# Performance work log

Hardware: AMD Instinct MI355X
Metric: run time of the kernel (lower is better)

## Reference

```python
import jax, jax.numpy as jnp
import numpy as np

N_NODES = 10000
EPS = 1e-5


def _layernorm(x, gamma, beta):
    mu = jnp.mean(x, axis=-1, keepdims=True)
    var = jnp.mean(jnp.square(x - mu), axis=-1, keepdims=True)
    return (x - mu) * jax.lax.rsqrt(var + EPS) * gamma + beta


def _sage_pool_layer(h, src, dst, Wp, bp, Ws, Wn, b, gamma, beta):
    # DGL SAGEConv(aggregator='pool'):
    #   m_u = relu(h_u @ Wp^T + bp); h_neigh[v] = max_{u in N(v)} m_u (0 if no neighbors)
    #   rst = h @ Ws^T + h_neigh @ Wn^T + b
    m = jax.nn.relu(h @ Wp.T + bp)              # [N, d]
    msg = m[src]                                 # [E, d] gather
    agg = jax.ops.segment_max(msg, dst, num_segments=N_NODES)
    agg = jnp.where(jnp.isfinite(agg), agg, 0.0)  # isolated nodes -> 0
    rst = h @ Ws.T + agg @ Wn.T + b
    # gsage_layer: LayerNorm, then Encoder applies relu (dropout inactive in eval)
    return jax.nn.relu(_layernorm(rst, gamma, beta))


def setup_inputs() -> dict:
    key = jax.random.key(0)
    ks = jax.random.split(key, 16)
    d = 256
    E = 320000
    s = 1.0 / np.sqrt(d)
    inp = {
        "h": jax.random.normal(ks[0], (N_NODES, d), dtype=jnp.float32),
        "edge_src": jax.random.randint(ks[1], (E,), 0, N_NODES, dtype=jnp.int32),
        "edge_dst": jax.random.randint(ks[2], (E,), 0, N_NODES, dtype=jnp.int32),
    }
    for li in range(2):
        kk = jax.random.split(ks[3 + li], 3)
        inp[f"Wp{li}"] = jax.random.normal(kk[0], (d, d), dtype=jnp.float32) * s
        inp[f"bp{li}"] = jnp.zeros((d,), jnp.float32)
        inp[f"Ws{li}"] = jax.random.normal(kk[1], (d, d), dtype=jnp.float32) * s
        inp[f"Wn{li}"] = jax.random.normal(kk[2], (d, d), dtype=jnp.float32) * s
        inp[f"b{li}"] = jnp.zeros((d,), jnp.float32)
        inp[f"g{li}"] = jnp.ones((d,), jnp.float32)
        inp[f"be{li}"] = jnp.zeros((d,), jnp.float32)
    return inp


def reference(h, edge_src, edge_dst,
              Wp0, bp0, Ws0, Wn0, b0, g0, be0,
              Wp1, bp1, Ws1, Wn1, b1, g1, be1):
    h = _sage_pool_layer(h, edge_src, edge_dst, Wp0, bp0, Ws0, Wn0, b0, g0, be0)
    h = _sage_pool_layer(h, edge_src, edge_dst, Wp1, bp1, Ws1, Wn1, b1, g1, be1)
    return h
```

## Files before the change

### kernel.cpp

```cpp
#include <hip/hip_runtime.h>

#define D 256
#define CAP 128
#define ASTRIDE 280
#define LN_EPS 1e-5f
#define MQ_ENC 32.0f
#define MQ_DEC 0.03125f

typedef short short8 __attribute__((ext_vector_type(8)));
typedef float floatx4 __attribute__((ext_vector_type(4)));
typedef unsigned short u16x8 __attribute__((ext_vector_type(8)));
typedef unsigned short us2 __attribute__((ext_vector_type(2)));

__device__ __forceinline__ unsigned short f2b(float f) {
    union { float f; unsigned int u; } x; x.f = f;
    unsigned int u = x.u + 0x7FFFu + ((x.u >> 16) & 1u);
    return (unsigned short)(u >> 16);
}

__device__ __forceinline__ unsigned bmax4(unsigned a, unsigned b) {
    union { unsigned u; us2 v; } al, bl, ah, bh, rl, rh;
    al.u = a & 0x00FF00FFu; bl.u = b & 0x00FF00FFu;
    ah.u = a & 0xFF00FF00u; bh.u = b & 0xFF00FF00u;
#if __has_builtin(__builtin_elementwise_max)
    rl.v = __builtin_elementwise_max(al.v, bl.v);
    rh.v = __builtin_elementwise_max(ah.v, bh.v);
#else
    rl.v[0] = al.v[0] > bl.v[0] ? al.v[0] : bl.v[0];
    rl.v[1] = al.v[1] > bl.v[1] ? al.v[1] : bl.v[1];
    rh.v[0] = ah.v[0] > bh.v[0] ? ah.v[0] : bh.v[0];
    rh.v[1] = ah.v[1] > bh.v[1] ? ah.v[1] : bh.v[1];
#endif
    return rl.u | rh.u;
}

__device__ __forceinline__ uint2 bmax8(uint2 a, uint2 b) {
    uint2 r; r.x = bmax4(a.x, b.x); r.y = bmax4(a.y, b.y); return r;
}

__device__ __forceinline__ unsigned char mq(float v) {
    return (unsigned char)(int)fminf(v * MQ_ENC + 0.5f, 255.0f);
}

__device__ __forceinline__ u16x8 deq8(uint2 x) {
    u16x8 r;
#pragma unroll
    for (int k = 0; k < 2; k++) {
        const unsigned w = k ? x.y : x.x;
#pragma unroll
        for (int j = 0; j < 4; j++)
            r[k * 4 + j] = f2b((float)((w >> (8 * j)) & 0xFFu) * MQ_DEC);
    }
    return r;
}

__global__ __launch_bounds__(256) void prep_kernel(
    const float* __restrict__ w0, const float* __restrict__ w1,
    const float* __restrict__ w2, const float* __restrict__ w3,
    const float* __restrict__ w4, const float* __restrict__ w5,
    unsigned short* __restrict__ wb,
    int* __restrict__ cnt, unsigned char* __restrict__ mb8,
    unsigned char* __restrict__ m1b8, int N)
{
    const int blk = blockIdx.x;
    const int tid = threadIdx.x;
    if (blk < 384) {
        const int wsel = blk >> 6;
        const float* src;
        switch (wsel) {
            case 0: src = w0; break; case 1: src = w1; break;
            case 2: src = w2; break; case 3: src = w3; break;
            case 4: src = w4; break; default: src = w5; break;
        }
        const int idx = (blk & 63) * 1024 + tid * 4;
        const float4 v = *(const float4*)(src + idx);
        ushort4 o;
        o.x = f2b(v.x); o.y = f2b(v.y); o.z = f2b(v.z); o.w = f2b(v.w);
        *(ushort4*)(wb + (size_t)wsel * 65536 + idx) = o;
    } else if (blk < 424) {
        const int i = (blk - 384) * 256 + tid;
        if (i < N) cnt[i] = 0;
    } else {
        mb8[(size_t)N * D + tid] = 0;
        m1b8[(size_t)N * D + tid] = 0;
    }
}

__global__ __launch_bounds__(256, 3) void relu_m(
    const float* __restrict__ h, const unsigned short* __restrict__ Wp,
    const float* __restrict__ bp, unsigned char* __restrict__ mb8,
    unsigned short* __restrict__ hb, int N,
    const int* __restrict__ esrc, const int* __restrict__ edst,
    int* __restrict__ cnt, unsigned short* __restrict__ csr, int E, int ngemm)
{
    if ((int)blockIdx.x >= ngemm) {
        const int nsb = gridDim.x - ngemm;
        int i = ((int)blockIdx.x - ngemm) * 256 + threadIdx.x;
        const int stride = nsb * 256;
        for (; i < E; i += stride) {
            const int d = edst[i];
            const int pos = atomicAdd(&cnt[d], 1);
            if (pos < CAP) csr[(size_t)d * CAP + pos] = (unsigned short)esrc[i];
        }
        return;
    }

    const int tid = threadIdx.x;
    const int wave = tid >> 6;
    const int lane = tid & 63;
    const int quad = lane >> 4;
    const int l16 = lane & 15;
    const int row0 = blockIdx.x * 16;
    const int koff = quad * 8;

    floatx4 acc[4];
#pragma unroll
    for (int t = 0; t < 4; t++) acc[t] = (floatx4)(0.f);

    const float* aptr = h + (size_t)(row0 + l16) * D + koff;
    const unsigned short* wptr = Wp + (size_t)(wave * 64 + l16) * D + koff;
#pragma unroll
    for (int k0 = 0; k0 < D; k0 += 32) {
        const float4 f0 = *(const float4*)(aptr + k0);
        const float4 f1 = *(const float4*)(aptr + k0 + 4);
        union { short8 s; ushort4 h[2]; } av;
        av.h[0].x = f2b(f0.x); av.h[0].y = f2b(f0.y);
        av.h[0].z = f2b(f0.z); av.h[0].w = f2b(f0.w);
        av.h[1].x = f2b(f1.x); av.h[1].y = f2b(f1.y);
        av.h[1].z = f2b(f1.z); av.h[1].w = f2b(f1.w);
        if (wave == 0)
            *(short8*)(hb + (size_t)(row0 + l16) * D + koff + k0) = av.s;
        const short8 b0 = *(const short8*)(wptr + k0);
        const short8 b1 = *(const short8*)(wptr + 16 * D + k0);
        const short8 b2 = *(const short8*)(wptr + 32 * D + k0);
        const short8 b3 = *(const short8*)(wptr + 48 * D + k0);
        acc[0] = __builtin_amdgcn_mfma_f32_16x16x32_bf16(av.s, b0, acc[0], 0, 0, 0);
        acc[1] = __builtin_amdgcn_mfma_f32_16x16x32_bf16(av.s, b1, acc[1], 0, 0, 0);
        acc[2] = __builtin_amdgcn_mfma_f32_16x16x32_bf16(av.s, b2, acc[2], 0, 0, 0);
        acc[3] = __builtin_amdgcn_mfma_f32_16x16x32_bf16(av.s, b3, acc[3], 0, 0, 0);
    }

#pragma unroll
    for (int t = 0; t < 4; t++) {
        const float bcol = bp[wave * 64 + t * 16 + l16];
#pragma unroll
        for (int r = 0; r < 4; r++) {
            const int rg = row0 + quad * 4 + r;
            const int col = wave * 64 + t * 16 + l16;
            mb8[(size_t)rg * D + col] = mq(fmaxf(acc[t][r] + bcol, 0.f));
        }
    }
}

__global__ __launch_bounds__(256, 3) void gemm_ln_pool(
    const unsigned short* __restrict__ A, const unsigned short* __restrict__ Wself,
    const unsigned short* __restrict__ Wneigh,
    const unsigned char* __restrict__ mpool,
    const int* __restrict__ cnt, const unsigned short* __restrict__ csr,
    const float* __restrict__ bias,
    const float* __restrict__ gamma, const float* __restrict__ beta,
    unsigned short* __restrict__ out_b, float* __restrict__ out_f,
    const unsigned short* __restrict__ Wnext, const float* __restrict__ bnext,
    unsigned char* __restrict__ mout, int N)
{
    __shared__ unsigned short idxS[16][CAP];
    __shared__ unsigned short aggS[16 * ASTRIDE];
    __shared__ float redS[4][16], redS2[4][16], muA[16], rsA[16];

    const int tid = threadIdx.x;
    const int wave = tid >> 6;
    const int lane = tid & 63;
    const int quad = lane >> 4;
    const int l16 = lane & 15;
    const int row0 = blockIdx.x * 16;
    const int koff = quad * 8;
    const int rbase = wave * 4;
    const int half = lane >> 5;
    const int l32 = lane & 31;

    int degs[4];
#pragma unroll
    for (int rr = 0; rr < 4; rr++) degs[rr] = min(cnt[row0 + rbase + rr], CAP);
    int P = max(max(degs[0], degs[1]), max(degs[2], degs[3]));
    const int P2R = (P + 7) & ~7;
#pragma unroll
    for (int rr = 0; rr < 4; rr++) {
        const int rg = row0 + rbase + rr;
        for (int i = lane; i < P2R; i += 64)
            idxS[rbase + rr][i] = (i < degs[rr]) ? csr[(size_t)rg * CAP + i]
                                                 : (unsigned short)N;
    }

    const int nb = P2R >> 1;
    const unsigned char* mbase = mpool + l32 * 8;

#define ISSUE_B(SL, bi)                                                         \
    {                                                                           \
        _Pragma("unroll") for (int rr = 0; rr < 4; rr++) {                      \
            const int jj = idxS[rbase + rr][2 * (bi) + half];                   \
            SL[rr] = *(const uint2*)(mbase + (size_t)jj * D);                   \
        }                                                                       \
    }
#define CONS_B(SL)                                                              \
    {                                                                           \
        _Pragma("unroll") for (int rr = 0; rr < 4; rr++)                        \
            mx[rr] = bmax8(mx[rr], SL[rr]);                                     \
    }

    uint2 g0[4], g1[4], g2[4], g3[4], mx[4];
#pragma unroll
    for (int rr = 0; rr < 4; rr++) mx[rr] = make_uint2(0u, 0u);

    if (nb) {
        ISSUE_B(g0, 0) ISSUE_B(g1, 1) ISSUE_B(g2, 2) ISSUE_B(g3, 3)
    }

    floatx4 acc[4];
#pragma unroll
    for (int t = 0; t < 4; t++) acc[t] = (floatx4)(0.f);

    {
        const unsigned short* aptr = A + (size_t)(row0 + l16) * D + koff;
        const unsigned short* wptr = Wself + (size_t)(wave * 64 + l16) * D + koff;
#pragma unroll
        for (int k0 = 0; k0 < D; k0 += 32) {
            const short8 av = *(const short8*)(aptr + k0);
            const short8 b0 = *(const short8*)(wptr + k0);
            const short8 b1 = *(const short8*)(wptr + 16 * D + k0);
            const short8 b2 = *(const short8*)(wptr + 32 * D + k0);
            const short8 b3 = *(const short8*)(wptr + 48 * D + k0);
            acc[0] = __builtin_amdgcn_mfma_f32_16x16x32_bf16(av, b0, acc[0], 0, 0, 0);
            acc[1] = __builtin_amdgcn_mfma_f32_16x16x32_bf16(av, b1, acc[1], 0, 0, 0);
            acc[2] = __builtin_amdgcn_mfma_f32_16x16x32_bf16(av, b2, acc[2], 0, 0, 0);
            acc[3] = __builtin_amdgcn_mfma_f32_16x16x32_bf16(av, b3, acc[3], 0, 0, 0);
        }
    }

    for (int b = 0; b < nb; b += 4) {
        const bool more = (b + 8 <= nb);
        CONS_B(g0) if (more) ISSUE_B(g0, b + 4)
        CONS_B(g1) if (more) ISSUE_B(g1, b + 5)
        CONS_B(g2) if (more) ISSUE_B(g2, b + 6)
        CONS_B(g3) if (more) ISSUE_B(g3, b + 7)
    }
#undef ISSUE_B
#undef CONS_B

#pragma unroll
    for (int rr = 0; rr < 4; rr++) {
        uint2 oth;
        oth.x = __shfl_xor((int)mx[rr].x, 32);
        oth.y = __shfl_xor((int)mx[rr].y, 32);
        const uint2 mf = bmax8(mx[rr], oth);
        if (half == 0)
            *(u16x8*)&aggS[(rbase + rr) * ASTRIDE + l32 * 8] = deq8(mf);
    }
    __syncthreads();

    {
        const unsigned short* wptr = Wneigh + (size_t)(wave * 64 + l16) * D + koff;
#pragma unroll
        for (int k0 = 0; k0 < D; k0 += 32) {
            const short8 av = *(const short8*)&aggS[l16 * ASTRIDE + koff + k0];
            const short8 b0 = *(const short8*)(wptr + k0);
            const short8 b1 = *(const short8*)(wptr + 16 * D + k0);
            const short8 b2 = *(const short8*)(wptr + 32 * D + k0);
            const short8 b3 = *(const short8*)(wptr + 48 * D + k0);
            acc[0] = __builtin_amdgcn_mfma_f32_16x16x32_bf16(av, b0, acc[0], 0, 0, 0);
            acc[1] = __builtin_amdgcn_mfma_f32_16x16x32_bf16(av, b1, acc[1], 0, 0, 0);
            acc[2] = __builtin_amdgcn_mfma_f32_16x16x32_bf16(av, b2, acc[2], 0, 0, 0);
            acc[3] = __builtin_amdgcn_mfma_f32_16x16x32_bf16(av, b3, acc[3], 0, 0, 0);
        }
    }

    float bcol[4];
#pragma unroll
    for (int t = 0; t < 4; t++) bcol[t] = bias[wave * 64 + t * 16 + l16];
#pragma unroll
    for (int t = 0; t < 4; t++)
#pragma unroll
        for (int r = 0; r < 4; r++) acc[t][r] += bcol[t];

#pragma unroll
    for (int r = 0; r < 4; r++) {
        float s = 0.f, s2 = 0.f;
#pragma unroll
        for (int t = 0; t < 4; t++) {
            const float v = acc[t][r];
            s += v; s2 += v * v;
        }
        s += __shfl_xor(s, 1);  s2 += __shfl_xor(s2, 1);
        s += __shfl_xor(s, 2);  s2 += __shfl_xor(s2, 2);
        s += __shfl_xor(s, 4);  s2 += __shfl_xor(s2, 4);
        s += __shfl_xor(s, 8);  s2 += __shfl_xor(s2, 8);
        if (l16 == 0) {
            redS[wave][quad * 4 + r] = s;
            redS2[wave][quad * 4 + r] = s2;
        }
    }
    __syncthreads();
    if (tid < 16) {
        const float S  = redS[0][tid] + redS[1][tid] + redS[2][tid] + redS[3][tid];
        const float S2 = redS2[0][tid] + redS2[1][tid] + redS2[2][tid] + redS2[3][tid];
        const float mu = S * (1.f / D);
        float var = S2 * (1.f / D) - mu * mu;
        var = fmaxf(var, 0.f);
        muA[tid] = mu;
        rsA[tid] = rsqrtf(var + LN_EPS);
    }
    __syncthreads();

    float gcol[4], becol[4];
#pragma unroll
    for (int t = 0; t < 4; t++) {
        gcol[t] = gamma[wave * 64 + t * 16 + l16];
        becol[t] = beta[wave * 64 + t * 16 + l16];
    }
#pragma unroll
    for (int r = 0; r < 4; r++) {
        const int rl = quad * 4 + r;
        const int rg = row0 + rl;
        const float mu = muA[rl];
        const float rs = rsA[rl];
#pragma unroll
        for (int t = 0; t < 4; t++) {
            const int col = wave * 64 + t * 16 + l16;
            float o = (acc[t][r] - mu) * rs * gcol[t] + becol[t];
            o = fmaxf(o, 0.f);
            const unsigned short ob = f2b(o);
            if (out_f) out_f[(size_t)rg * D + col] = o;
            else       out_b[(size_t)rg * D + col] = ob;
            if (Wnext) aggS[rl * ASTRIDE + col] = ob;
        }
    }

    if (Wnext) {
        __syncthreads();
#pragma unroll
        for (int t = 0; t < 4; t++) acc[t] = (floatx4)(0.f);
        const unsigned short* wptr = Wnext + (size_t)(wave * 64 + l16) * D + koff;
#pragma unroll
        for (int k0 = 0; k0 < D; k0 += 32) {
            const short8 av = *(const short8*)&aggS[l16 * ASTRIDE + koff + k0];
            const short8 b0 = *(const short8*)(wptr + k0);
            const short8 b1 = *(const short8*)(wptr + 16 * D + k0);
            const short8 b2 = *(const short8*)(wptr + 32 * D + k0);
            const short8 b3 = *(const short8*)(wptr + 48 * D + k0);
            acc[0] = __builtin_amdgcn_mfma_f32_16x16x32_bf16(av, b0, acc[0], 0, 0, 0);
            acc[1] = __builtin_amdgcn_mfma_f32_16x16x32_bf16(av, b1, acc[1], 0, 0, 0);
            acc[2] = __builtin_amdgcn_mfma_f32_16x16x32_bf16(av, b2, acc[2], 0, 0, 0);
            acc[3] = __builtin_amdgcn_mfma_f32_16x16x32_bf16(av, b3, acc[3], 0, 0, 0);
        }
#pragma unroll
        for (int t = 0; t < 4; t++) {
            const float bc = bnext[wave * 64 + t * 16 + l16];
#pragma unroll
            for (int r = 0; r < 4; r++) {
                const int rg = row0 + quad * 4 + r;
                const int col = wave * 64 + t * 16 + l16;
                mout[(size_t)rg * D + col] = mq(fmaxf(acc[t][r] + bc, 0.f));
            }
        }
    }
}

extern "C" void kernel_launch(void* const* d_in, const int* in_sizes, int n_in,
                              void* d_out, int out_size, void* d_ws, size_t ws_size,
                              hipStream_t stream) {
    const float* h    = (const float*)d_in[0];
    const int*   esrc = (const int*)d_in[1];
    const int*   edst = (const int*)d_in[2];
    const float* Wp0  = (const float*)d_in[3];
    const float* bp0  = (const float*)d_in[4];
    const float* Ws0  = (const float*)d_in[5];
    const float* Wn0  = (const float*)d_in[6];
    const float* b0   = (const float*)d_in[7];
    const float* g0   = (const float*)d_in[8];
    const float* be0  = (const float*)d_in[9];
    const float* Wp1  = (const float*)d_in[10];
    const float* bp1  = (const float*)d_in[11];
    const float* Ws1  = (const float*)d_in[12];
    const float* Wn1  = (const float*)d_in[13];
    const float* b1   = (const float*)d_in[14];
    const float* g1   = (const float*)d_in[15];
    const float* be1  = (const float*)d_in[16];

    const int N = in_sizes[0] / D;
    const int E = in_sizes[1];
    const size_t ND = (size_t)N * D;

    unsigned short* hb  = (unsigned short*)d_ws;
    unsigned short* h1b = hb + ND;
    unsigned short* wb  = h1b + ND;
    int* cnt = (int*)(wb + 6 * 65536);
    unsigned short* csr = (unsigned short*)(cnt + N);
    unsigned char* mb8  = (unsigned char*)(csr + (size_t)N * CAP);
    unsigned char* m1b8 = mb8 + ND + D;

    unsigned short* wpb0 = wb + 0 * 65536;
    unsigned short* wsb0 = wb + 1 * 65536;
    unsigned short* wnb0 = wb + 2 * 65536;
    unsigned short* wpb1 = wb + 3 * 65536;
    unsigned short* wsb1 = wb + 4 * 65536;
    unsigned short* wnb1 = wb + 5 * 65536;

    const int gblocks = N / 16;
    const int sblocks = 1024;

    prep_kernel<<<425, 256, 0, stream>>>(Wp0, Ws0, Wn0, Wp1, Ws1, Wn1, wb,
                                         cnt, mb8, m1b8, N);

    relu_m<<<gblocks + sblocks, 256, 0, stream>>>(h, wpb0, bp0, mb8, hb, N,
                                                  esrc, edst, cnt, csr, E, gblocks);
    gemm_ln_pool<<<gblocks, 256, 0, stream>>>(hb, wsb0, wnb0, mb8, cnt, csr,
                                              b0, g0, be0, h1b, nullptr,
                                              wpb1, bp1, m1b8, N);

    gemm_ln_pool<<<gblocks, 256, 0, stream>>>(h1b, wsb1, wnb1, m1b8, cnt, csr,
                                              b1, g1, be1, nullptr, (float*)d_out,
                                              nullptr, nullptr, nullptr, N);
}
```

Baseline: 213.5 us.

## Fuse both SAGE layers into one persistent kernel with a grid barrier

After: 406.2 us. 90.3% more time.

```diff
diff --git a/kernel.cpp b/kernel.cpp
--- a/kernel.cpp
+++ b/kernel.cpp
@@ -60,7 +60,7 @@
     const float* __restrict__ w4, const float* __restrict__ w5,
     unsigned short* __restrict__ wb,
     int* __restrict__ cnt, unsigned char* __restrict__ mb8,
-    unsigned char* __restrict__ m1b8, int N)
+    unsigned char* __restrict__ m1b8, unsigned* __restrict__ bar, int N)
 {
     const int blk = blockIdx.x;
     const int tid = threadIdx.x;
@@ -83,6 +83,7 @@
     } else {
         mb8[(size_t)N * D + tid] = 0;
         m1b8[(size_t)N * D + tid] = 0;
+        if (tid == 0) *bar = 0u;
     }
 }
 
@@ -152,19 +153,23 @@
     }
 }
 
-__global__ __launch_bounds__(256, 3) void gemm_ln_pool(
-    const unsigned short* __restrict__ A, const unsigned short* __restrict__ Wself,
-    const unsigned short* __restrict__ Wneigh,
-    const unsigned char* __restrict__ mpool,
+__global__ __launch_bounds__(256, 3) void lnpool2(
+    const unsigned short* __restrict__ A0,
+    const unsigned short* __restrict__ Ws0, const unsigned short* __restrict__ Wn0,
+    const unsigned char* __restrict__ m0,
     const int* __restrict__ cnt, const unsigned short* __restrict__ csr,
-    const float* __restrict__ bias,
-    const float* __restrict__ gamma, const float* __restrict__ beta,
-    unsigned short* __restrict__ out_b, float* __restrict__ out_f,
-    const unsigned short* __restrict__ Wnext, const float* __restrict__ bnext,
-    unsigned char* __restrict__ mout, int N)
+    const float* __restrict__ b0v, const float* __restrict__ g0v,
+    const float* __restrict__ be0v,
+    const unsigned short* __restrict__ Wp1, const float* __restrict__ bp1v,
+    unsigned char* __restrict__ m1,
+    const unsigned short* __restrict__ Ws1, const unsigned short* __restrict__ Wn1,
+    const float* __restrict__ b1v, const float* __restrict__ g1v,
+    const float* __restrict__ be1v,
+    float* __restrict__ outf, unsigned* __restrict__ bar, int N)
 {
     __shared__ unsigned short idxS[16][CAP];
-    __shared__ unsigned short aggS[16 * ASTRIDE];
+    __shared__ unsigned short aggA[16 * ASTRIDE];
+    __shared__ unsigned short aggB[16 * ASTRIDE];
     __shared__ float redS[4][16], redS2[4][16], muA[16], rsA[16];
 
     const int tid = threadIdx.x;
@@ -190,15 +195,13 @@
             idxS[rbase + rr][i] = (i < degs[rr]) ? csr[(size_t)rg * CAP + i]
                                                  : (unsigned short)N;
     }
-
     const int nb = P2R >> 1;
-    const unsigned char* mbase = mpool + l32 * 8;
-
-#define ISSUE_B(SL, bi)                                                         \
+
+#define ISSUE_B(SRC, SL, bi)                                                    \
     {                                                                           \
         _Pragma("unroll") for (int rr = 0; rr < 4; rr++) {                      \
             const int jj = idxS[rbase + rr][2 * (bi) + half];                   \
-            SL[rr] = *(const uint2*)(mbase + (size_t)jj * D);                   \
+            SL[rr] = *(const uint2*)((SRC) + (size_t)jj * D + l32 * 8);         \
         }                                                                       \
     }
 #define CONS_B(SL)                                                              \
@@ -206,120 +209,107 @@
         _Pragma("unroll") for (int rr = 0; rr < 4; rr++)                        \
             mx[rr] = bmax8(mx[rr], SL[rr]);                                     \
     }
+#define POOL_CONSUME(SRC)                                                       \
+    for (int b = 0; b < nb; b += 4) {                                           \
+        const bool more = (b + 8 <= nb);                                        \
+        CONS_B(g0) if (more) ISSUE_B(SRC, g0, b + 4)                            \
+        CONS_B(g1) if (more) ISSUE_B(SRC, g1, b + 5)                            \
+        CONS_B(g2) if (more) ISSUE_B(SRC, g2, b + 6)                            \
+        CONS_B(g3) if (more) ISSUE_B(SRC, g3, b + 7)                            \
+    }
+#define POOL_PARK()                                                             \
+    _Pragma("unroll") for (int rr = 0; rr < 4; rr++) {                          \
+        uint2 oth;                                                              \
+        oth.x = __shfl_xor((int)mx[rr].x, 32);                                  \
+        oth.y = __shfl_xor((int)mx[rr].y, 32);                                  \
+        const uint2 mf = bmax8(mx[rr], oth);                                    \
+        if (half == 0)                                                          \
+            *(u16x8*)&aggA[(rbase + rr) * ASTRIDE + l32 * 8] = deq8(mf);        \
+    }
+#define GEMM_GLB(APTR, WMAT)                                                    \
+    {                                                                           \
+        const unsigned short* wptr = (WMAT) + (size_t)(wave * 64 + l16) * D + koff; \
+        _Pragma("unroll") for (int k0 = 0; k0 < D; k0 += 32) {                  \
+            const short8 av = *(const short8*)((APTR) + k0);                    \
+            const short8 b0 = *(const short8*)(wptr + k0);                      \
+            const short8 b1 = *(const short8*)(wptr + 16 * D + k0);             \
+            const short8 b2 = *(const short8*)(wptr + 32 * D + k0);             \
+            const short8 b3 = *(const short8*)(wptr + 48 * D + k0);             \
+            acc[0] = __builtin_amdgcn_mfma_f32_16x16x32_bf16(av, b0, acc[0], 0, 0, 0); \
+            acc[1] = __builtin_amdgcn_mfma_f32_16x16x32_bf16(av, b1, acc[1], 0, 0, 0); \
+            acc[2] = __builtin_amdgcn_mfma_f32_16x16x32_bf16(av, b2, acc[2], 0, 0, 0); \
+            acc[3] = __builtin_amdgcn_mfma_f32_16x16x32_bf16(av, b3, acc[3], 0, 0, 0); \
+        }                                                                       \
+    }
+#define GEMM_LDS(ABUF, WMAT)                                                    \
+    {                                                                           \
+        const unsigned short* wptr = (WMAT) + (size_t)(wave * 64 + l16) * D + koff; \
+        _Pragma("unroll") for (int k0 = 0; k0 < D; k0 += 32) {                  \
+            const short8 av = *(const short8*)&(ABUF)[l16 * ASTRIDE + koff + k0]; \
+            const short8 b0 = *(const short8*)(wptr + k0);                      \
+            const short8 b1 = *(const short8*)(wptr + 16 * D + k0);             \
+            const short8 b2 = *(const short8*)(wptr + 32 * D + k0);             \
+            const short8 b3 = *(const short8*)(wptr + 48 * D + k0);             \
+            acc[0] = __builtin_amdgcn_mfma_f32_16x16x32_bf16(av, b0, acc[0], 0, 0, 0); \
+            acc[1] = __builtin_amdgcn_mfma_f32_16x16x32_bf16(av, b1, acc[1], 0, 0, 0); \
+            acc[2] = __builtin_amdgcn_mfma_f32_16x16x32_bf16(av, b2, acc[2], 0, 0, 0); \
+            acc[3] = __builtin_amdgcn_mfma_f32_16x16x32_bf16(av, b3, acc[3], 0, 0, 0); \
+        }                                                                       \
+    }
+#define LN_REDUCE(GV, BEV)                                                      \
+    _Pragma("unroll") for (int r = 0; r < 4; r++) {                             \
+        float s = 0.f, s2 = 0.f;                                                \
+        _Pragma("unroll") for (int t = 0; t < 4; t++) {                         \
+            const float v = acc[t][r]; s += v; s2 += v * v;                     \
+        }                                                                       \
+        s += __shfl_xor(s, 1);  s2 += __shfl_xor(s2, 1);                        \
+        s += __shfl_xor(s, 2);  s2 += __shfl_xor(s2, 2);                        \
+        s += __shfl_xor(s, 4);  s2 += __shfl_xor(s2, 4);                        \
+        s += __shfl_xor(s, 8);  s2 += __shfl_xor(s2, 8);                        \
+        if (l16 == 0) { redS[wave][quad * 4 + r] = s; redS2[wave][quad * 4 + r] = s2; } \
+    }                                                                           \
+    __syncthreads();                                                            \
+    if (tid < 16) {                                                             \
+        const float S  = redS[0][tid] + redS[1][tid] + redS[2][tid] + redS[3][tid];   \
+        const float S2 = redS2[0][tid] + redS2[1][tid] + redS2[2][tid] + redS2[3][tid]; \
+        const float mu = S * (1.f / D);                                         \
+        float var = S2 * (1.f / D) - mu * mu;                                   \
+        var = fmaxf(var, 0.f);                                                  \
+        muA[tid] = mu; rsA[tid] = rsqrtf(var + LN_EPS);                         \
+    }                                                                           \
+    __syncthreads();                                                            \
+    float gcol[4], becol[4];                                                    \
+    _Pragma("unroll") for (int t = 0; t < 4; t++) {                             \
+        gcol[t] = (GV)[wave * 64 + t * 16 + l16];                               \
+        becol[t] = (BEV)[wave * 64 + t * 16 + l16];                             \
+    }
 
     uint2 g0[4], g1[4], g2[4], g3[4], mx[4];
 #pragma unroll
     for (int rr = 0; rr < 4; rr++) mx[rr] = make_uint2(0u, 0u);
 
-    if (nb) {
-        ISSUE_B(g0, 0) ISSUE_B(g1, 1) ISSUE_B(g2, 2) ISSUE_B(g3, 3)
-    }
+    if (nb) { ISSUE_B(m0, g0, 0) ISSUE_B(m0, g1, 1) ISSUE_B(m0, g2, 2) ISSUE_B(m0, g3, 3) }
 
     floatx4 acc[4];
 #pragma unroll
     for (int t = 0; t < 4; t++) acc[t] = (floatx4)(0.f);
 
-    {
-        const unsigned short* aptr = A + (size_t)(row0 + l16) * D + koff;
-        const unsigned short* wptr = Wself + (size_t)(wave * 64 + l16) * D + koff;
-#pragma unroll
-        for (int k0 = 0; k0 < D; k0 += 32) {
-            const short8 av = *(const short8*)(aptr + k0);
-            const short8 b0 = *(const short8*)(wptr + k0);
-            const short8 b1 = *(const short8*)(wptr + 16 * D + k0);
-            const short8 b2 = *(const short8*)(wptr + 32 * D + k0);
-            const short8 b3 = *(const short8*)(wptr + 48 * D + k0);
-            acc[0] = __builtin_amdgcn_mfma_f32_16x16x32_bf16(av, b0, acc[0], 0, 0, 0);
-            acc[1] = __builtin_amdgcn_mfma_f32_16x16x32_bf16(av, b1, acc[1], 0, 0, 0);
-            acc[2] = __builtin_amdgcn_mfma_f32_16x16x32_bf16(av, b2, acc[2], 0, 0, 0);
-            acc[3] = __builtin_amdgcn_mfma_f32_16x16x32_bf16(av, b3, acc[3], 0, 0, 0);
-        }
-    }
-
-    for (int b = 0; b < nb; b += 4) {
-        const bool more = (b + 8 <= nb);
-        CONS_B(g0) if (more) ISSUE_B(g0, b + 4)
-        CONS_B(g1) if (more) ISSUE_B(g1, b + 5)
-        CONS_B(g2) if (more) ISSUE_B(g2, b + 6)
-        CONS_B(g3) if (more) ISSUE_B(g3, b + 7)
-    }
-#undef ISSUE_B
-#undef CONS_B
-
-#pragma unroll
-    for (int rr = 0; rr < 4; rr++) {
-        uint2 oth;
-        oth.x = __shfl_xor((int)mx[rr].x, 32);
-        oth.y = __shfl_xor((int)mx[rr].y, 32);
-        const uint2 mf = bmax8(mx[rr], oth);
-        if (half == 0)
-            *(u16x8*)&aggS[(rbase + rr) * ASTRIDE + l32 * 8] = deq8(mf);
-    }
+    GEMM_GLB(A0 + (size_t)(row0 + l16) * D + koff, Ws0)
+    POOL_CONSUME(m0)
+    POOL_PARK()
     __syncthreads();
-
-    {
-        const unsigned short* wptr = Wneigh + (size_t)(wave * 64 + l16) * D + koff;
-#pragma unroll
-        for (int k0 = 0; k0 < D; k0 += 32) {
-            const short8 av = *(const short8*)&aggS[l16 * ASTRIDE + koff + k0];
-            const short8 b0 = *(const short8*)(wptr + k0);
-            const short8 b1 = *(const short8*)(wptr + 16 * D + k0);
-            const short8 b2 = *(const short8*)(wptr + 32 * D + k0);
-            const short8 b3 = *(const short8*)(wptr + 48 * D + k0);
-            acc[0] = __builtin_amdgcn_mfma_f32_16x16x32_bf16(av, b0, acc[0], 0, 0, 0);
-            acc[1] = __builtin_amdgcn_mfma_f32_16x16x32_bf16(av, b1, acc[1], 0, 0, 0);
-            acc[2] = __builtin_amdgcn_mfma_f32_16x16x32_bf16(av, b2, acc[2], 0, 0, 0);
-            acc[3] = __builtin_amdgcn_mfma_f32_16x16x32_bf16(av, b3, acc[3], 0, 0, 0);
-        }
-    }
-
-    float bcol[4];
-#pragma unroll
-    for (int t = 0; t < 4; t++) bcol[t] = bias[wave * 64 + t * 16 + l16];
-#pragma unroll
-    for (int t = 0; t < 4; t++)
-#pragma unroll
-        for (int r = 0; r < 4; r++) acc[t][r] += bcol[t];
-
-#pragma unroll
-    for (int r = 0; r < 4; r++) {
-        float s = 0.f, s2 = 0.f;
-#pragma unroll
-        for (int t = 0; t < 4; t++) {
-            const float v = acc[t][r];
-            s += v; s2 += v * v;
-        }
-        s += __shfl_xor(s, 1);  s2 += __shfl_xor(s2, 1);
-        s += __shfl_xor(s, 2);  s2 += __shfl_xor(s2, 2);
-        s += __shfl_xor(s, 4);  s2 += __shfl_xor(s2, 4);
-        s += __shfl_xor(s, 8);  s2 += __shfl_xor(s2, 8);
-        if (l16 == 0) {
-            redS[wave][quad * 4 + r] = s;
-            redS2[wave][quad * 4 + r] = s2;
-        }
-    }
-    __syncthreads();
-    if (tid < 16) {
-        const float S  = redS[0][tid] + redS[1][tid] + redS[2][tid] + redS[3][tid];
-        const float S2 = redS2[0][tid] + redS2[1][tid] + redS2[2][tid] + redS2[3][tid];
-        const float mu = S * (1.f / D);
-        float var = S2 * (1.f / D) - mu * mu;
-        var = fmaxf(var, 0.f);
-        muA[tid] = mu;
-        rsA[tid] = rsqrtf(var + LN_EPS);
-    }
-    __syncthreads();
-
-    float gcol[4], becol[4];
+    GEMM_LDS(aggA, Wn0)
+
 #pragma unroll
     for (int t = 0; t < 4; t++) {
-        gcol[t] = gamma[wave * 64 + t * 16 + l16];
-        becol[t] = beta[wave * 64 + t * 16 + l16];
-    }
+        const float bc = b0v[wave * 64 + t * 16 + l16];
+#pragma unroll
+        for (int r = 0; r < 4; r++) acc[t][r] += bc;
+    }
+    LN_REDUCE(g0v, be0v)
 #pragma unroll
     for (int r = 0; r < 4; r++) {
         const int rl = quad * 4 + r;
-        const int rg = row0 + rl;
         const float mu = muA[rl];
         const float rs = rsA[rl];
 #pragma unroll
@@ -327,41 +317,78 @@
             const int col = wave * 64 + t * 16 + l16;
             float o = (acc[t][r] - mu) * rs * gcol[t] + becol[t];
             o = fmaxf(o, 0.f);
-            const unsigned short ob = f2b(o);
-            if (out_f) out_f[(size_t)rg * D + col] = o;
-            else       out_b[(size_t)rg * D + col] = ob;
-            if (Wnext) aggS[rl * ASTRIDE + col] = ob;
-        }
-    }
-
-    if (Wnext) {
-        __syncthreads();
-#pragma unroll
-        for (int t = 0; t < 4; t++) acc[t] = (floatx4)(0.f);
-        const unsigned short* wptr = Wnext + (size_t)(wave * 64 + l16) * D + koff;
-#pragma unroll
-        for (int k0 = 0; k0 < D; k0 += 32) {
-            const short8 av = *(const short8*)&aggS[l16 * ASTRIDE + koff + k0];
-            const short8 b0 = *(const short8*)(wptr + k0);
-            const short8 b1 = *(const short8*)(wptr + 16 * D + k0);
-            const short8 b2 = *(const short8*)(wptr + 32 * D + k0);
-            const short8 b3 = *(const short8*)(wptr + 48 * D + k0);
-            acc[0] = __builtin_amdgcn_mfma_f32_16x16x32_bf16(av, b0, acc[0], 0, 0, 0);
-            acc[1] = __builtin_amdgcn_mfma_f32_16x16x32_bf16(av, b1, acc[1], 0, 0, 0);
-            acc[2] = __builtin_amdgcn_mfma_f32_16x16x32_bf16(av, b2, acc[2], 0, 0, 0);
-            acc[3] = __builtin_amdgcn_mfma_f32_16x16x32_bf16(av, b3, acc[3], 0, 0, 0);
-        }
-#pragma unroll
-        for (int t = 0; t < 4; t++) {
-            const float bc = bnext[wave * 64 + t * 16 + l16];
-#pragma unroll
-            for (int r = 0; r < 4; r++) {
-                const int rg = row0 + quad * 4 + r;
+            aggB[rl * ASTRIDE + col] = f2b(o);
+        }
+    }
+    __syncthreads();
+
+#pragma unroll
+    for (int t = 0; t < 4; t++) acc[t] = (floatx4)(0.f);
+    GEMM_LDS(aggB, Wp1)
+#pragma unroll
+    for (int t = 0; t < 4; t++) {
+        const float bc = bp1v[wave * 64 + t * 16 + l16];
+#pragma unroll
+        for (int r = 0; r < 4; r++) {
+            const int rg = row0 + quad * 4 + r;
+            const int col = wave * 64 + t * 16 + l16;
+            m1[(size_t)rg * D + col] = mq(fmaxf(acc[t][r] + bc, 0.f));
+        }
+    }
+
+    __syncthreads();
+    if (tid == 0) {
+        __threadfence();
+        __hip_atomic_fetch_add(bar, 1u, __ATOMIC_ACQ_REL, __HIP_MEMORY_SCOPE_AGENT);
+        while (__hip_atomic_load(bar, __ATOMIC_ACQUIRE, __HIP_MEMORY_SCOPE_AGENT)
+               < (unsigned)gridDim.x)
+            __builtin_amdgcn_s_sleep(16);
+    }
+    __syncthreads();
+    __threadfence();
+
+#pragma unroll
+    for (int rr = 0; rr < 4; rr++) mx[rr] = make_uint2(0u, 0u);
+    if (nb) { ISSUE_B(m1, g0, 0) ISSUE_B(m1, g1, 1) ISSUE_B(m1, g2, 2) ISSUE_B(m1, g3, 3) }
+
+#pragma unroll
+    for (int t = 0; t < 4; t++) acc[t] = (floatx4)(0.f);
+
+    GEMM_LDS(aggB, Ws1)
+    POOL_CONSUME(m1)
+    POOL_PARK()
+    __syncthreads();
+    GEMM_LDS(aggA, Wn1)
+
+#pragma unroll
+    for (int t = 0; t < 4; t++) {
+        const float bc = b1v[wave * 64 + t * 16 + l16];
+#pragma unroll
+        for (int r = 0; r < 4; r++) acc[t][r] += bc;
+    }
+    {
+        LN_REDUCE(g1v, be1v)
+#pragma unroll
+        for (int r = 0; r < 4; r++) {
+            const int rl = quad * 4 + r;
+            const int rg = row0 + rl;
+            const float mu = muA[rl];
+            const float rs = rsA[rl];
+#pragma unroll
+            for (int t = 0; t < 4; t++) {
                 const int col = wave * 64 + t * 16 + l16;
-                mout[(size_t)rg * D + col] = mq(fmaxf(acc[t][r] + bc, 0.f));
+                float o = (acc[t][r] - mu) * rs * gcol[t] + becol[t];
+                outf[(size_t)rg * D + col] = fmaxf(o, 0.f);
             }
         }
     }
+#undef ISSUE_B
+#undef CONS_B
+#undef POOL_CONSUME
+#undef POOL_PARK
+#undef GEMM_GLB
+#undef GEMM_LDS
+#undef LN_REDUCE
 }
 
 extern "C" void kernel_launch(void* const* d_in, const int* in_sizes, int n_in,
@@ -390,12 +417,12 @@
     const size_t ND = (size_t)N * D;
 
     unsigned short* hb  = (unsigned short*)d_ws;
-    unsigned short* h1b = hb + ND;
-    unsigned short* wb  = h1b + ND;
+    unsigned short* wb  = hb + ND;
     int* cnt = (int*)(wb + 6 * 65536);
     unsigned short* csr = (unsigned short*)(cnt + N);
     unsigned char* mb8  = (unsigned char*)(csr + (size_t)N * CAP);
     unsigned char* m1b8 = mb8 + ND + D;
+    unsigned* bar = (unsigned*)(m1b8 + ND + D);
 
     unsigned short* wpb0 = wb + 0 * 65536;
     unsigned short* wsb0 = wb + 1 * 65536;
@@ -408,15 +435,13 @@
     const int sblocks = 1024;
 
     prep_kernel<<<425, 256, 0, stream>>>(Wp0, Ws0, Wn0, Wp1, Ws1, Wn1, wb,
-                                         cnt, mb8, m1b8, N);
+                                         cnt, mb8, m1b8, bar, N);
 
     relu_m<<<gblocks + sblocks, 256, 0, stream>>>(h, wpb0, bp0, mb8, hb, N,
                                                   esrc, edst, cnt, csr, E, gblocks);
-    gemm_ln_pool<<<gblocks, 256, 0, stream>>>(hb, wsb0, wnb0, mb8, cnt, csr,
-                                              b0, g0, be0, h1b, nullptr,
-                                              wpb1, bp1, m1b8, N);
-
-    gemm_ln_pool<<<gblocks, 256, 0, stream>>>(h1b, wsb1, wnb1, m1b8, cnt, csr,
-                                              b1, g1, be1, nullptr, (float*)d_out,
-                                              nullptr, nullptr, nullptr, N);
-}
+
+    lnpool2<<<gblocks, 256, 0, stream>>>(hb, wsb0, wnb0, mb8, cnt, csr,
+                                         b0, g0, be0, wpb1, bp1, m1b8,
+                                         wsb1, wnb1, b1, g1, be1,
+                                         (float*)d_out, bar, N);
+}
```
